# Performance work log

Hardware: AMD Instinct MI355X
Metric: run time of the kernel (lower is better)

Reference implementation:

```python
import jax, jax.numpy as jnp
import numpy as np

WS = (7, 7)          # window size
NUM_HEADS = 4
DIM = 128
B_ = 4096            # batch * num_windows
NW = 256             # num windows per image (mask leading dim)
N = WS[0] * WS[1]    # 49 tokens per window


def _relative_position_index(ws):
    coords = np.stack(np.meshgrid(np.arange(ws[0]), np.arange(ws[1]), indexing='ij'))
    coords = coords.reshape(2, -1)                      # [2, N]
    rel = coords[:, :, None] - coords[:, None, :]       # [2, N, N]
    rel = rel.transpose(1, 2, 0).astype(np.int64)       # [N, N, 2]
    rel[:, :, 0] += ws[0] - 1
    rel[:, :, 1] += ws[1] - 1
    rel[:, :, 0] *= 2 * ws[1] - 1
    return rel.sum(-1)                                  # [N, N] in [0, (2w-1)^2)

REL_POS_INDEX = jnp.asarray(_relative_position_index(WS))


def setup_inputs() -> dict:
    key = jax.random.key(0)
    ks = jax.random.split(key, 4)
    x = jax.random.normal(ks[0], (B_, N, DIM), dtype=jnp.float32)
    mask = jnp.zeros((NW, N, N), dtype=jnp.float32)
    qkv_w = jax.random.normal(ks[1], (DIM, 3 * DIM), dtype=jnp.float32) * 0.02
    qkv_b = jnp.zeros((3 * DIM,), dtype=jnp.float32)
    proj_w = jax.random.normal(ks[2], (DIM, DIM), dtype=jnp.float32) * 0.02
    proj_b = jnp.zeros((DIM,), dtype=jnp.float32)
    bias_table = jax.random.normal(ks[3], ((2 * WS[0] - 1) * (2 * WS[1] - 1), NUM_HEADS), dtype=jnp.float32) * 0.02
    return {"x": x, "mask": mask, "qkv_w": qkv_w, "qkv_b": qkv_b,
            "proj_w": proj_w, "proj_b": proj_b, "bias_table": bias_table}


def reference(x, mask, qkv_w, qkv_b, proj_w, proj_b, bias_table):
    B, n, C = x.shape
    H = NUM_HEADS
    hd = C // H
    scale = hd ** (-0.5)

    qkv = x @ qkv_w + qkv_b                            # [B, N, 3C]
    qkv = qkv.reshape(B, n, 3, H, hd).transpose(2, 0, 3, 1, 4)  # [3, B, H, N, hd]
    q, k, v = qkv[0], qkv[1], qkv[2]

    attn = jnp.einsum('bhnd,bhmd->bhnm', q * scale, k)  # [B, H, N, N]

    # gathered relative-position bias: [N*N, H] -> [H, N, N]
    bias = bias_table[REL_POS_INDEX.reshape(-1)].reshape(n, n, H).transpose(2, 0, 1)
    attn = attn + bias[None]

    nW = mask.shape[0]
    attn = attn.reshape(-1, nW, H, n, n) + mask[None, :, None].astype(attn.dtype)
    attn = attn.reshape(-1, H, n, n)
    attn = jax.nn.softmax(attn, axis=-1)

    out = jnp.einsum('bhnm,bhmd->bnhd', attn, v).reshape(B, n, C)
    out = out @ proj_w + proj_b
    return out
```

## Files before the change

kernel.cpp:

```cpp
#include <hip/hip_runtime.h>
#include <hip/hip_bf16.h>


typedef __attribute__((ext_vector_type(8))) short bf16x8;
typedef __attribute__((ext_vector_type(4))) float f32x4;

#define NTOK  49
#define CDIM  128
#define NWIN  256
#define SCALE 0.17677669529663687f
#define PROJ_WOFF 49152

static __device__ __forceinline__ unsigned pk2(float a, float b) {
    __hip_bfloat162 h = __float22bfloat162_rn(make_float2(a, b));
    unsigned u; __builtin_memcpy(&u, &h, 4); return u;
}
static __device__ __forceinline__ short bf1(float a) {
    __hip_bfloat16 h = __float2bfloat16(a);
    unsigned short u; __builtin_memcpy(&u, &h, 2); return (short)u;
}
static __device__ __forceinline__ bf16x8 repack(unsigned p00, unsigned p01,
                                                unsigned p10, unsigned p11,
                                                int src0, int src1, bool hi) {
    union { bf16x8 v; unsigned u[4]; } t;
    unsigned a0, a1;
    a0 = __shfl((int)p00, src0, 64); a1 = __shfl((int)p10, src0, 64); t.u[0] = hi ? a1 : a0;
    a0 = __shfl((int)p01, src0, 64); a1 = __shfl((int)p11, src0, 64); t.u[1] = hi ? a1 : a0;
    a0 = __shfl((int)p00, src1, 64); a1 = __shfl((int)p10, src1, 64); t.u[2] = hi ? a1 : a0;
    a0 = __shfl((int)p01, src1, 64); a1 = __shfl((int)p11, src1, 64); t.u[3] = hi ? a1 : a0;
    return t.v;
}

__global__ void prep_w(const float* __restrict__ qkv_w,
                       const float* __restrict__ proj_w,
                       short* __restrict__ wb) {
    const int fid = blockIdx.x;
    const int l   = threadIdx.x;
    const int lq = l & 15, lg = l >> 4;
    bf16x8 v;
    if (fid < 96) {
        const int nt = fid >> 2, kk = fid & 3;
        #pragma unroll
        for (int j = 0; j < 8; ++j)
            v[j] = bf1(qkv_w[(kk*32 + lg*8 + j)*384 + nt*16 + lq]);
        *(bf16x8*)(wb + fid*512 + l*8) = v;
    } else {
        const int f2 = fid - 96;
        const int nt = f2 >> 2, kk = f2 & 3;
        #pragma unroll
        for (int j = 0; j < 8; ++j)
            v[j] = bf1(proj_w[(kk*32 + lg*8 + j)*128 + nt*16 + lq]);
        *(bf16x8*)(wb + PROJ_WOFF + f2*512 + l*8) = v;
    }
}

__global__ __launch_bounds__(256, 5)
void win_attn(const float* __restrict__ x,
              const float* __restrict__ mask,
              const float* __restrict__ qkv_b,
              const float* __restrict__ proj_b,
              const float* __restrict__ bias_table,
              const short* __restrict__ wb,
              float* __restrict__ out) {
    __shared__ __align__(16) short kl[64 * 128];
    __shared__ __align__(16) short vt[128 * 64];

    const int b    = blockIdx.x;
    const int tid  = threadIdx.x;
    const int l    = tid & 63;
    const int wave = tid >> 6;
    const int lq   = l & 15, lg = l >> 4;
    const int m0   = wave * 16;
    const int qtok = m0 + lq;

    const float* xb = x + (size_t)b * (NTOK * CDIM);
    bf16x8 xa[4];
    {
        int row = qtok; if (row > 48) row = 48;
        const float* pr = xb + row*CDIM + lg*8;
        #pragma unroll
        for (int kk = 0; kk < 4; ++kk) {
            float4 f0 = *(const float4*)(pr + kk*32);
            float4 f1 = *(const float4*)(pr + kk*32 + 4);
            union { bf16x8 v; unsigned u[4]; } t;
            t.u[0] = pk2(f0.x, f0.y);
            t.u[1] = pk2(f0.z, f0.w);
            t.u[2] = pk2(f1.x, f1.y);
            t.u[3] = pk2(f1.z, f1.w);
            xa[kk] = t.v;
        }
    }

    unsigned qpk[8][2];
    #pragma unroll
    for (int nt = 0; nt < 24; ++nt) {
        bf16x8 wf[4];
        #pragma unroll
        for (int kk = 0; kk < 4; ++kk)
            wf[kk] = *(const bf16x8*)(wb + (nt*4 + kk)*512 + l*8);
        f32x4 acc = *(const f32x4*)(qkv_b + nt*16 + lg*4);
        #pragma unroll
        for (int kk = 0; kk < 4; ++kk)
            acc = __builtin_amdgcn_mfma_f32_16x16x32_bf16(wf[kk], xa[kk], acc, 0, 0, 0);
        if (nt < 8) {
            qpk[nt][0] = pk2(acc[0]*SCALE, acc[1]*SCALE);
            qpk[nt][1] = pk2(acc[2]*SCALE, acc[3]*SCALE);
        } else if (nt < 16) {
            unsigned w0 = pk2(acc[0], acc[1]);
            unsigned w1 = pk2(acc[2], acc[3]);
            const int ub  = (nt - 8)*2 + (lg >> 1);
            const int off = qtok*128 + ((ub ^ (qtok & 7)) << 3) + (lg & 1)*4;
            *(unsigned long long*)(kl + off) =
                (unsigned long long)w0 | ((unsigned long long)w1 << 32);
        } else {
            #pragma unroll
            for (int r = 0; r < 4; ++r) {
                const int dim = (nt - 16)*16 + lg*4 + r;
                vt[dim*64 + (((qtok >> 3) ^ (dim & 7)) << 3) + (qtok & 7)] = bf1(acc[r]);
            }
        }
    }

    const float* mwin = mask + (size_t)(b & (NWIN - 1)) * (NTOK * NTOK);
    unsigned bmpk[4][4][2];
    {
        const unsigned NEG = pk2(-1e30f, -1e30f);
        #pragma unroll
        for (int nt = 0; nt < 4; ++nt)
            #pragma unroll
            for (int r = 0; r < 4; ++r) {
                const int kt = nt*16 + lg*4 + r;
                if (qtok < NTOK && kt < NTOK) {
                    const int ridx = (qtok/7 - kt/7 + 6)*13 + (qtok%7 - kt%7 + 6);
                    const f32x4 b4 = *(const f32x4*)(bias_table + ridx*4);
                    const float mv = mwin[qtok*NTOK + kt];
                    bmpk[nt][r][0] = pk2(b4[0] + mv, b4[1] + mv);
                    bmpk[nt][r][1] = pk2(b4[2] + mv, b4[3] + mv);
                } else {
                    bmpk[nt][r][0] = NEG; bmpk[nt][r][1] = NEG;
                }
            }
    }
    __syncthreads();

    const int src0 = lq + 16*((2*lg + 0) & 3);
    const int src1 = lq + 16*((2*lg + 1) & 3);
    const bool hi  = (lg >> 1);
    unsigned aopk[8][2];

    #pragma unroll
    for (int h = 0; h < 4; ++h) {
        const bf16x8 qf = repack(qpk[2*h][0], qpk[2*h][1], qpk[2*h+1][0], qpk[2*h+1][1],
                                 src0, src1, hi);
        f32x4 s[4];
        #pragma unroll
        for (int nt = 0; nt < 4; ++nt) {
            const int krow = nt*16 + lq;
            const int u    = h*4 + lg;
            bf16x8 kf = *(const bf16x8*)(kl + krow*128 + ((u ^ (krow & 7)) << 3));
            f32x4 z = {0.f, 0.f, 0.f, 0.f};
            s[nt] = __builtin_amdgcn_mfma_f32_16x16x32_bf16(kf, qf, z, 0, 0, 0);
        }
        #pragma unroll
        for (int nt = 0; nt < 4; ++nt)
            #pragma unroll
            for (int r = 0; r < 4; ++r) {
                const unsigned u = bmpk[nt][r][h >> 1];
                const float bm = __uint_as_float((h & 1) ? (u & 0xffff0000u) : (u << 16));
                s[nt][r] += bm;
            }
        float mx;
        {
            float m_[4];
            #pragma unroll
            for (int nt = 0; nt < 4; ++nt)
                m_[nt] = fmaxf(fmaxf(s[nt][0], s[nt][1]), fmaxf(s[nt][2], s[nt][3]));
            mx = fmaxf(fmaxf(m_[0], m_[1]), fmaxf(m_[2], m_[3]));
        }
        mx = fmaxf(mx, __shfl_xor(mx, 16, 64));
        mx = fmaxf(mx, __shfl_xor(mx, 32, 64));
        float sum;
        {
            float s_[4];
            #pragma unroll
            for (int nt = 0; nt < 4; ++nt) {
                #pragma unroll
                for (int r = 0; r < 4; ++r)
                    s[nt][r] = __expf(s[nt][r] - mx);
                s_[nt] = (s[nt][0] + s[nt][1]) + (s[nt][2] + s[nt][3]);
            }
            sum = (s_[0] + s_[1]) + (s_[2] + s_[3]);
        }
        sum += __shfl_xor(sum, 16, 64);
        sum += __shfl_xor(sum, 32, 64);
        const float inv = 1.0f / sum;
        unsigned pkv[4][2];
        #pragma unroll
        for (int nt = 0; nt < 4; ++nt) {
            pkv[nt][0] = pk2(s[nt][0]*inv, s[nt][1]*inv);
            pkv[nt][1] = pk2(s[nt][2]*inv, s[nt][3]*inv);
        }
        bf16x8 pa[2];
        #pragma unroll
        for (int c = 0; c < 2; ++c)
            pa[c] = repack(pkv[2*c][0], pkv[2*c][1], pkv[2*c+1][0], pkv[2*c+1][1],
                           src0, src1, hi);
        #pragma unroll
        for (int dn = 0; dn < 2; ++dn) {
            f32x4 o = {0.f, 0.f, 0.f, 0.f};
            #pragma unroll
            for (int kk = 0; kk < 2; ++kk) {
                const int dim = h*32 + dn*16 + lq;
                const int u   = kk*4 + lg;
                bf16x8 vf = *(const bf16x8*)(vt + dim*64 + ((u ^ (dim & 7)) << 3));
                o = __builtin_amdgcn_mfma_f32_16x16x32_bf16(vf, pa[kk], o, 0, 0, 0);
            }
            aopk[2*h + dn][0] = pk2(o[0], o[1]);
            aopk[2*h + dn][1] = pk2(o[2], o[3]);
        }
    }

    bf16x8 ab[4];
    #pragma unroll
    for (int kk = 0; kk < 4; ++kk)
        ab[kk] = repack(aopk[2*kk][0], aopk[2*kk][1], aopk[2*kk+1][0], aopk[2*kk+1][1],
                        src0, src1, hi);
    float* ob = out + (size_t)b * (NTOK * CDIM);
    #pragma unroll
    for (int nt = 0; nt < 8; ++nt) {
        bf16x8 wf[4];
        #pragma unroll
        for (int kk = 0; kk < 4; ++kk)
            wf[kk] = *(const bf16x8*)(wb + PROJ_WOFF + (nt*4 + kk)*512 + l*8);
        f32x4 acc = *(const f32x4*)(proj_b + nt*16 + lg*4);
        #pragma unroll
        for (int kk = 0; kk < 4; ++kk)
            acc = __builtin_amdgcn_mfma_f32_16x16x32_bf16(wf[kk], ab[kk], acc, 0, 0, 0);
        if (qtok < NTOK)
            *(f32x4*)(ob + qtok*CDIM + nt*16 + lg*4) = acc;
    }
}

extern "C" void kernel_launch(void* const* d_in, const int* in_sizes, int n_in,
                              void* d_out, int out_size, void* d_ws, size_t ws_size,
                              hipStream_t stream) {
    (void)in_sizes; (void)n_in; (void)out_size; (void)ws_size;
    const float* x          = (const float*)d_in[0];
    const float* mask       = (const float*)d_in[1];
    const float* qkv_w      = (const float*)d_in[2];
    const float* qkv_b      = (const float*)d_in[3];
    const float* proj_w     = (const float*)d_in[4];
    const float* proj_b     = (const float*)d_in[5];
    const float* bias_table = (const float*)d_in[6];
    float* out = (float*)d_out;
    short* wb  = (short*)d_ws;

    hipLaunchKernelGGL(prep_w,   dim3(128),  dim3(64),  0, stream, qkv_w, proj_w, wb);
    hipLaunchKernelGGL(win_attn, dim3(4096), dim3(256), 0, stream,
                       x, mask, qkv_b, proj_b, bias_table, wb, out);
}
```

Measured before the change: 132.8 us.

## Interleave pairs of QKV tiles and attention heads for ILP; fold scale into weights

Q scaling moves into the one-time weight conversion: the Q weight columns are pre-multiplied, and the Q bias is scaled before the MFMA chain, so the per-element multiply on the Q accumulators goes away. The QKV projection loop now processes two output tiles per iteration, and attention processes two heads at once, interleaving their MFMAs, reductions and shuffles. The goal is more independent work per wave to hide MFMA and shuffle latency. In exchange, register pressure rises and the occupancy hint drops from 5 to 4 blocks per CU.

```diff
diff --git a/kernel.cpp b/kernel.cpp
--- a/kernel.cpp
+++ b/kernel.cpp
@@ -40,9 +40,10 @@
     bf16x8 v;
     if (fid < 96) {
         const int nt = fid >> 2, kk = fid & 3;
+        const float s = (fid < 32) ? SCALE : 1.0f;
         #pragma unroll
         for (int j = 0; j < 8; ++j)
-            v[j] = bf1(qkv_w[(kk*32 + lg*8 + j)*384 + nt*16 + lq]);
+            v[j] = bf1(qkv_w[(kk*32 + lg*8 + j)*384 + nt*16 + lq] * s);
         *(bf16x8*)(wb + fid*512 + l*8) = v;
     } else {
         const int f2 = fid - 96;
@@ -54,7 +55,7 @@
     }
 }
 
-__global__ __launch_bounds__(256, 5)
+__global__ __launch_bounds__(256, 4)
 void win_attn(const float* __restrict__ x,
               const float* __restrict__ mask,
               const float* __restrict__ qkv_b,
@@ -93,30 +94,44 @@
 
     unsigned qpk[8][2];
     #pragma unroll
-    for (int nt = 0; nt < 24; ++nt) {
-        bf16x8 wf[4];
-        #pragma unroll
-        for (int kk = 0; kk < 4; ++kk)
-            wf[kk] = *(const bf16x8*)(wb + (nt*4 + kk)*512 + l*8);
-        f32x4 acc = *(const f32x4*)(qkv_b + nt*16 + lg*4);
-        #pragma unroll
-        for (int kk = 0; kk < 4; ++kk)
-            acc = __builtin_amdgcn_mfma_f32_16x16x32_bf16(wf[kk], xa[kk], acc, 0, 0, 0);
-        if (nt < 8) {
-            qpk[nt][0] = pk2(acc[0]*SCALE, acc[1]*SCALE);
-            qpk[nt][1] = pk2(acc[2]*SCALE, acc[3]*SCALE);
-        } else if (nt < 16) {
-            unsigned w0 = pk2(acc[0], acc[1]);
-            unsigned w1 = pk2(acc[2], acc[3]);
-            const int ub  = (nt - 8)*2 + (lg >> 1);
-            const int off = qtok*128 + ((ub ^ (qtok & 7)) << 3) + (lg & 1)*4;
-            *(unsigned long long*)(kl + off) =
-                (unsigned long long)w0 | ((unsigned long long)w1 << 32);
-        } else {
-            #pragma unroll
-            for (int r = 0; r < 4; ++r) {
-                const int dim = (nt - 16)*16 + lg*4 + r;
-                vt[dim*64 + (((qtok >> 3) ^ (dim & 7)) << 3) + (qtok & 7)] = bf1(acc[r]);
+    for (int np = 0; np < 12; ++np) {
+        const int n0 = 2*np, n1 = 2*np + 1;
+        bf16x8 wfA[4], wfB[4];
+        #pragma unroll
+        for (int kk = 0; kk < 4; ++kk)
+            wfA[kk] = *(const bf16x8*)(wb + (n0*4 + kk)*512 + l*8);
+        #pragma unroll
+        for (int kk = 0; kk < 4; ++kk)
+            wfB[kk] = *(const bf16x8*)(wb + (n1*4 + kk)*512 + l*8);
+        f32x4 aA = *(const f32x4*)(qkv_b + n0*16 + lg*4);
+        f32x4 aB = *(const f32x4*)(qkv_b + n1*16 + lg*4);
+        if (n0 < 8) { aA = aA * SCALE; aB = aB * SCALE; }
+        #pragma unroll
+        for (int kk = 0; kk < 4; ++kk)
+            aA = __builtin_amdgcn_mfma_f32_16x16x32_bf16(wfA[kk], xa[kk], aA, 0, 0, 0);
+        #pragma unroll
+        for (int kk = 0; kk < 4; ++kk)
+            aB = __builtin_amdgcn_mfma_f32_16x16x32_bf16(wfB[kk], xa[kk], aB, 0, 0, 0);
+        #pragma unroll
+        for (int e = 0; e < 2; ++e) {
+            const int nt = 2*np + e;
+            const f32x4 acc = e ? aB : aA;
+            if (nt < 8) {
+                qpk[nt][0] = pk2(acc[0], acc[1]);
+                qpk[nt][1] = pk2(acc[2], acc[3]);
+            } else if (nt < 16) {
+                unsigned w0 = pk2(acc[0], acc[1]);
+                unsigned w1 = pk2(acc[2], acc[3]);
+                const int ub  = (nt - 8)*2 + (lg >> 1);
+                const int off = qtok*128 + ((ub ^ (qtok & 7)) << 3) + (lg & 1)*4;
+                *(unsigned long long*)(kl + off) =
+                    (unsigned long long)w0 | ((unsigned long long)w1 << 32);
+            } else {
+                #pragma unroll
+                for (int r = 0; r < 4; ++r) {
+                    const int dim = (nt - 16)*16 + lg*4 + r;
+                    vt[dim*64 + (((qtok >> 3) ^ (dim & 7)) << 3) + (qtok & 7)] = bf1(acc[r]);
+                }
             }
         }
     }
@@ -149,74 +164,100 @@
     unsigned aopk[8][2];
 
     #pragma unroll
-    for (int h = 0; h < 4; ++h) {
-        const bf16x8 qf = repack(qpk[2*h][0], qpk[2*h][1], qpk[2*h+1][0], qpk[2*h+1][1],
-                                 src0, src1, hi);
-        f32x4 s[4];
+    for (int hp = 0; hp < 2; ++hp) {
+        const int h0 = 2*hp, h1 = h0 + 1;
+        const bf16x8 qfA = repack(qpk[2*h0][0], qpk[2*h0][1], qpk[2*h0+1][0], qpk[2*h0+1][1],
+                                  src0, src1, hi);
+        const bf16x8 qfB = repack(qpk[2*h1][0], qpk[2*h1][1], qpk[2*h1+1][0], qpk[2*h1+1][1],
+                                  src0, src1, hi);
+        f32x4 sA[4], sB[4];
         #pragma unroll
         for (int nt = 0; nt < 4; ++nt) {
             const int krow = nt*16 + lq;
-            const int u    = h*4 + lg;
-            bf16x8 kf = *(const bf16x8*)(kl + krow*128 + ((u ^ (krow & 7)) << 3));
+            bf16x8 kfA = *(const bf16x8*)(kl + krow*128 + (((h0*4 + lg) ^ (krow & 7)) << 3));
+            bf16x8 kfB = *(const bf16x8*)(kl + krow*128 + (((h1*4 + lg) ^ (krow & 7)) << 3));
             f32x4 z = {0.f, 0.f, 0.f, 0.f};
-            s[nt] = __builtin_amdgcn_mfma_f32_16x16x32_bf16(kf, qf, z, 0, 0, 0);
+            sA[nt] = __builtin_amdgcn_mfma_f32_16x16x32_bf16(kfA, qfA, z, 0, 0, 0);
+            sB[nt] = __builtin_amdgcn_mfma_f32_16x16x32_bf16(kfB, qfB, z, 0, 0, 0);
         }
         #pragma unroll
         for (int nt = 0; nt < 4; ++nt)
             #pragma unroll
             for (int r = 0; r < 4; ++r) {
-                const unsigned u = bmpk[nt][r][h >> 1];
-                const float bm = __uint_as_float((h & 1) ? (u & 0xffff0000u) : (u << 16));
-                s[nt][r] += bm;
-            }
-        float mx;
+                const unsigned u = bmpk[nt][r][hp];
+                sA[nt][r] += __uint_as_float(u << 16);
+                sB[nt][r] += __uint_as_float(u & 0xffff0000u);
+            }
+        float mxA, mxB;
         {
-            float m_[4];
-            #pragma unroll
-            for (int nt = 0; nt < 4; ++nt)
-                m_[nt] = fmaxf(fmaxf(s[nt][0], s[nt][1]), fmaxf(s[nt][2], s[nt][3]));
-            mx = fmaxf(fmaxf(m_[0], m_[1]), fmaxf(m_[2], m_[3]));
-        }
-        mx = fmaxf(mx, __shfl_xor(mx, 16, 64));
-        mx = fmaxf(mx, __shfl_xor(mx, 32, 64));
-        float sum;
+            float a_[4], b_[4];
+            #pragma unroll
+            for (int nt = 0; nt < 4; ++nt) {
+                a_[nt] = fmaxf(fmaxf(sA[nt][0], sA[nt][1]), fmaxf(sA[nt][2], sA[nt][3]));
+                b_[nt] = fmaxf(fmaxf(sB[nt][0], sB[nt][1]), fmaxf(sB[nt][2], sB[nt][3]));
+            }
+            mxA = fmaxf(fmaxf(a_[0], a_[1]), fmaxf(a_[2], a_[3]));
+            mxB = fmaxf(fmaxf(b_[0], b_[1]), fmaxf(b_[2], b_[3]));
+        }
+        mxA = fmaxf(mxA, __shfl_xor(mxA, 16, 64));
+        mxB = fmaxf(mxB, __shfl_xor(mxB, 16, 64));
+        mxA = fmaxf(mxA, __shfl_xor(mxA, 32, 64));
+        mxB = fmaxf(mxB, __shfl_xor(mxB, 32, 64));
+        float sumA, sumB;
         {
-            float s_[4];
+            float a_[4], b_[4];
             #pragma unroll
             for (int nt = 0; nt < 4; ++nt) {
                 #pragma unroll
-                for (int r = 0; r < 4; ++r)
-                    s[nt][r] = __expf(s[nt][r] - mx);
-                s_[nt] = (s[nt][0] + s[nt][1]) + (s[nt][2] + s[nt][3]);
-            }
-            sum = (s_[0] + s_[1]) + (s_[2] + s_[3]);
-        }
-        sum += __shfl_xor(sum, 16, 64);
-        sum += __shfl_xor(sum, 32, 64);
-        const float inv = 1.0f / sum;
-        unsigned pkv[4][2];
+                for (int r = 0; r < 4; ++r) {
+                    sA[nt][r] = __expf(sA[nt][r] - mxA);
+                    sB[nt][r] = __expf(sB[nt][r] - mxB);
+                }
+                a_[nt] = (sA[nt][0] + sA[nt][1]) + (sA[nt][2] + sA[nt][3]);
+                b_[nt] = (sB[nt][0] + sB[nt][1]) + (sB[nt][2] + sB[nt][3]);
+            }
+            sumA = (a_[0] + a_[1]) + (a_[2] + a_[3]);
+            sumB = (b_[0] + b_[1]) + (b_[2] + b_[3]);
+        }
+        sumA += __shfl_xor(sumA, 16, 64);
+        sumB += __shfl_xor(sumB, 16, 64);
+        sumA += __shfl_xor(sumA, 32, 64);
+        sumB += __shfl_xor(sumB, 32, 64);
+        const float invA = 1.0f / sumA;
+        const float invB = 1.0f / sumB;
+        unsigned pkvA[4][2], pkvB[4][2];
         #pragma unroll
         for (int nt = 0; nt < 4; ++nt) {
-            pkv[nt][0] = pk2(s[nt][0]*inv, s[nt][1]*inv);
-            pkv[nt][1] = pk2(s[nt][2]*inv, s[nt][3]*inv);
-        }
-        bf16x8 pa[2];
-        #pragma unroll
-        for (int c = 0; c < 2; ++c)
-            pa[c] = repack(pkv[2*c][0], pkv[2*c][1], pkv[2*c+1][0], pkv[2*c+1][1],
-                           src0, src1, hi);
+            pkvA[nt][0] = pk2(sA[nt][0]*invA, sA[nt][1]*invA);
+            pkvA[nt][1] = pk2(sA[nt][2]*invA, sA[nt][3]*invA);
+            pkvB[nt][0] = pk2(sB[nt][0]*invB, sB[nt][1]*invB);
+            pkvB[nt][1] = pk2(sB[nt][2]*invB, sB[nt][3]*invB);
+        }
+        bf16x8 paA[2], paB[2];
+        #pragma unroll
+        for (int c = 0; c < 2; ++c) {
+            paA[c] = repack(pkvA[2*c][0], pkvA[2*c][1], pkvA[2*c+1][0], pkvA[2*c+1][1],
+                            src0, src1, hi);
+            paB[c] = repack(pkvB[2*c][0], pkvB[2*c][1], pkvB[2*c+1][0], pkvB[2*c+1][1],
+                            src0, src1, hi);
+        }
         #pragma unroll
         for (int dn = 0; dn < 2; ++dn) {
-            f32x4 o = {0.f, 0.f, 0.f, 0.f};
+            f32x4 oA = {0.f, 0.f, 0.f, 0.f};
+            f32x4 oB = {0.f, 0.f, 0.f, 0.f};
             #pragma unroll
             for (int kk = 0; kk < 2; ++kk) {
-                const int dim = h*32 + dn*16 + lq;
-                const int u   = kk*4 + lg;
-                bf16x8 vf = *(const bf16x8*)(vt + dim*64 + ((u ^ (dim & 7)) << 3));
-                o = __builtin_amdgcn_mfma_f32_16x16x32_bf16(vf, pa[kk], o, 0, 0, 0);
-            }
-            aopk[2*h + dn][0] = pk2(o[0], o[1]);
-            aopk[2*h + dn][1] = pk2(o[2], o[3]);
+                const int dimA = h0*32 + dn*16 + lq;
+                const int dimB = h1*32 + dn*16 + lq;
+                bf16x8 vfA = *(const bf16x8*)(vt + dimA*64 + (((kk*4 + lg) ^ (dimA & 7)) << 3));
+                bf16x8 vfB = *(const bf16x8*)(vt + dimB*64 + (((kk*4 + lg) ^ (dimB & 7)) << 3));
+                oA = __builtin_amdgcn_mfma_f32_16x16x32_bf16(vfA, paA[kk], oA, 0, 0, 0);
+                oB = __builtin_amdgcn_mfma_f32_16x16x32_bf16(vfB, paB[kk], oB, 0, 0, 0);
+            }
+            aopk[2*h0 + dn][0] = pk2(oA[0], oA[1]);
+            aopk[2*h0 + dn][1] = pk2(oA[2], oA[3]);
+            aopk[2*h1 + dn][0] = pk2(oB[0], oB[1]);
+            aopk[2*h1 + dn][1] = pk2(oB[2], oB[3]);
         }
     }
 
```

New measurement: 131.2 us. No clear change (-1.3%).
